# Kernel optimization log

Hardware: AMD Instinct MI355X
Metric: run time of the kernel (lower is better)

The kernel has to match this reference:

```python
import jax, jax.numpy as jnp
import numpy as np
import math

B, S, D, H = 2, 2048, 1024, 16

def setup_inputs() -> dict:
    key = jax.random.key(0)
    ks = jax.random.split(key, 13)
    def lin(kw, kb, out_d, in_d):
        W = jax.random.normal(kw, (out_d, in_d), dtype=jnp.float32) * 0.02
        b = jax.random.normal(kb, (out_d,), dtype=jnp.float32) * 0.02
        return W, b
    Wq, bq = lin(ks[0], ks[1], D, D)
    Wk, bk = lin(ks[2], ks[3], D, D)
    Wv, bv = lin(ks[4], ks[5], D, D)
    Wo, bo = lin(ks[6], ks[7], D, D)
    query = jax.random.normal(ks[8], (B, S, D), dtype=jnp.float32)
    key_t = jax.random.normal(ks[9], (B, S, D), dtype=jnp.float32)
    value = jax.random.normal(ks[10], (B, S, D), dtype=jnp.float32)
    src_mask = jax.random.randint(ks[11], (B, S), 0, 2).astype(bool)  # True = masked out
    return {"query": query, "key": key_t, "value": value, "src_mask": src_mask,
            "Wq": Wq, "bq": bq, "Wk": Wk, "bk": bk, "Wv": Wv, "bv": bv,
            "Wo": Wo, "bo": bo, "nhead": H}

def reference(query, key, value, src_mask, Wq, bq, Wk, bk, Wv, bv, Wo, bo, nhead):
    b, s, d = query.shape
    hd = d // nhead
    scale = 1.0 / math.sqrt(hd)
    def split_heads(x):  # [b,s,d] -> [b,h,s,hd]
        return x.reshape(b, -1, nhead, hd).transpose(0, 2, 1, 3)
    q = split_heads(query @ Wq.T + bq)
    k = split_heads(key @ Wk.T + bk)
    v = split_heads(value @ Wv.T + bv)
    scores = jnp.einsum('bhqe,bhke->bhqk', q, k) * scale  # [b,h,s,s]
    # mask True -> -9e9, broadcast over heads and query positions (matches repeat)
    scores = jnp.where(src_mask[:, None, None, :], jnp.float32(-9e9), scores)
    probs = jax.nn.softmax(scores, axis=-1)
    # dropout is identity in eval mode
    out = jnp.einsum('bhqk,bhke->bhqe', probs, v)  # [b,h,s,hd]
    out = out.transpose(0, 2, 1, 3).reshape(b, s, d)
    out = out @ Wo.T + bo
    return out
```

## Files before the change

kernel.cpp:

```cpp
#include <hip/hip_runtime.h>
#include <hip/hip_bf16.h>
#include <cstdint>
#include <cstddef>

#define B_ 2
#define S_ 2048
#define D_ 1024
#define H_ 16
#define HD_ 64
#define M_ 4096

typedef __attribute__((ext_vector_type(8))) short short8;
typedef __attribute__((ext_vector_type(4))) short shortx4;
typedef __attribute__((ext_vector_type(4))) float floatx4;

__device__ __forceinline__ floatx4 mfma32(short8 a, short8 b, floatx4 c) {
    return __builtin_amdgcn_mfma_f32_16x16x32_bf16(a, b, c, 0, 0, 0);
}
__device__ __forceinline__ floatx4 mfma16(shortx4 a, shortx4 b, floatx4 c) {
    return __builtin_amdgcn_mfma_f32_16x16x16bf16_1k(a, b, c, 0, 0, 0);
}

__device__ __forceinline__ void gload_lds16(const __hip_bfloat16* g, __hip_bfloat16* lds_base) {
    __builtin_amdgcn_global_load_lds(
        (const __attribute__((address_space(1))) void*)g,
        (__attribute__((address_space(3))) void*)lds_base, 16, 0, 0);
}

__global__ __launch_bounds__(256) void cvt3_kernel(
    const float* __restrict__ a, const float* __restrict__ b, const float* __restrict__ c,
    __hip_bfloat16* __restrict__ dst, int n)
{
    const float* src = blockIdx.z == 0 ? a : blockIdx.z == 1 ? b : c;
    __hip_bfloat16* d = dst + (size_t)blockIdx.z * n;
    int i = (blockIdx.x * 256 + threadIdx.x) * 4;
    float4 v = *(const float4*)(src + i);
    union { __hip_bfloat16 h[4]; uint2 u; } cv;
    cv.h[0] = __float2bfloat16(v.x); cv.h[1] = __float2bfloat16(v.y);
    cv.h[2] = __float2bfloat16(v.z); cv.h[3] = __float2bfloat16(v.w);
    *(uint2*)(d + i) = cv.u;
}

__global__ __launch_bounds__(256) void cvt4_kernel(
    const float* __restrict__ a, const float* __restrict__ b,
    const float* __restrict__ c, const float* __restrict__ e,
    __hip_bfloat16* __restrict__ dst, int n)
{
    const float* src = blockIdx.z == 0 ? a : blockIdx.z == 1 ? b : blockIdx.z == 2 ? c : e;
    __hip_bfloat16* d = dst + (size_t)blockIdx.z * n;
    int i = (blockIdx.x * 256 + threadIdx.x) * 4;
    float4 v = *(const float4*)(src + i);
    union { __hip_bfloat16 h[4]; uint2 u; } cv;
    cv.h[0] = __float2bfloat16(v.x); cv.h[1] = __float2bfloat16(v.y);
    cv.h[2] = __float2bfloat16(v.z); cv.h[3] = __float2bfloat16(v.w);
    *(uint2*)(d + i) = cv.u;
}

template <int MODE>
__device__ __forceinline__ void gemm_core(
    const __hip_bfloat16* __restrict__ A,
    const __hip_bfloat16* __restrict__ W,
    const float* __restrict__ bias,
    void* __restrict__ Cout,
    __hip_bfloat16* __restrict__ smem,
    int m0, int n0, int N)
{
    __hip_bfloat16* As = smem;
    __hip_bfloat16* Bs = smem + 128 * 32;
    const int K = D_;
    const int tid  = threadIdx.x;
    const int wave = tid >> 6;
    const int lane = tid & 63;
    const int quad = lane >> 4;
    const int l15  = lane & 15;
    const int wm   = (wave & 1) * 64;
    const int wn   = (wave >> 1) * 64;
    const int srow = lane >> 2;
    const int scol = (lane & 3) * 8;

    floatx4 acc[4][4];
#pragma unroll
    for (int i = 0; i < 4; i++)
#pragma unroll
        for (int j = 0; j < 4; j++) {
            floatx4 z = {0.f, 0.f, 0.f, 0.f};
            acc[i][j] = z;
        }

    for (int k0 = 0; k0 < K; k0 += 32) {
        __syncthreads();
#pragma unroll
        for (int t = 0; t < 2; t++) {
            int r0 = wave * 32 + t * 16;
            gload_lds16(A + (size_t)(m0 + r0 + srow) * K + k0 + scol, As + r0 * 32);
            gload_lds16(W + (size_t)(n0 + r0 + srow) * K + k0 + scol, Bs + r0 * 32);
        }
        __syncthreads();

        short8 afr[4], bfr[4];
#pragma unroll
        for (int i = 0; i < 4; i++)
            afr[i] = *(const short8*)(As + (wm + i * 16 + l15) * 32 + quad * 8);
#pragma unroll
        for (int j = 0; j < 4; j++)
            bfr[j] = *(const short8*)(Bs + (wn + j * 16 + l15) * 32 + quad * 8);
#pragma unroll
        for (int i = 0; i < 4; i++)
#pragma unroll
            for (int j = 0; j < 4; j++)
                acc[i][j] = mfma32(afr[i], bfr[j], acc[i][j]);
    }

    if constexpr (MODE == 1) {
#pragma unroll
        for (int j = 0; j < 4; j++) {
            int col = n0 + wn + j * 16 + l15;
            int h = col >> 6, e = col & 63;
            float bv = bias[col];
#pragma unroll
            for (int i = 0; i < 4; i++) {
                int s0 = m0 + wm + i * 16 + quad * 4;
                int bb = s0 >> 11, sl = s0 & 2047;
                union { __hip_bfloat16 hx[4]; uint2 u; } pk;
#pragma unroll
                for (int r = 0; r < 4; r++)
                    pk.hx[r] = __float2bfloat16(acc[i][j][r] + bv);
                *(uint2*)((__hip_bfloat16*)Cout + (((size_t)bb * H_ + h) * HD_ + e) * S_ + sl) = pk.u;
            }
        }
    } else {
#pragma unroll
        for (int j = 0; j < 4; j++) {
            int col = n0 + wn + j * 16 + l15;
            float bv = bias[col];
#pragma unroll
            for (int i = 0; i < 4; i++) {
#pragma unroll
                for (int r = 0; r < 4; r++) {
                    int rowg = m0 + wm + i * 16 + quad * 4 + r;
                    ((__hip_bfloat16*)Cout)[(size_t)rowg * N + col] =
                        __float2bfloat16(acc[i][j][r] + bv);
                }
            }
        }
    }
}

__global__ __launch_bounds__(256) void qkv_gemm_kernel(
    const __hip_bfloat16* __restrict__ qb, const __hip_bfloat16* __restrict__ kb,
    const __hip_bfloat16* __restrict__ vb,
    const __hip_bfloat16* __restrict__ Wqb, const __hip_bfloat16* __restrict__ Wkb,
    const __hip_bfloat16* __restrict__ Wvb,
    const float* __restrict__ bq, const float* __restrict__ bk, const float* __restrict__ bv,
    __hip_bfloat16* __restrict__ Qp, __hip_bfloat16* __restrict__ Kp,
    __hip_bfloat16* __restrict__ Vt)
{
    __shared__ __hip_bfloat16 smem[2 * 128 * 32] __attribute__((aligned(16)));
    const int z = blockIdx.z;
    const __hip_bfloat16* A = z == 0 ? qb : z == 1 ? kb : vb;
    const __hip_bfloat16* W = z == 0 ? Wqb : z == 1 ? Wkb : Wvb;
    const float* bias = z == 0 ? bq : z == 1 ? bk : bv;
    int m0 = blockIdx.y * 128, n0 = blockIdx.x * 128;
    if (z < 2) gemm_core<0>(A, W, bias, z == 0 ? (void*)Qp : (void*)Kp, smem, m0, n0, D_);
    else       gemm_core<1>(A, W, bias, (void*)Vt, smem, m0, n0, D_);
}

__global__ __launch_bounds__(256) void oproj_gemm_kernel(
    const __hip_bfloat16* __restrict__ A, const __hip_bfloat16* __restrict__ W,
    const float* __restrict__ bias, float* __restrict__ out)
{
    __shared__ __hip_bfloat16 As[64 * 32]  __attribute__((aligned(16)));
    __shared__ __hip_bfloat16 Bs[128 * 32] __attribute__((aligned(16)));
    const int K = D_, N = D_;
    const int tid  = threadIdx.x;
    const int m0   = blockIdx.y * 64;
    const int n0   = blockIdx.x * 128;
    const int wave = tid >> 6;
    const int lane = tid & 63;
    const int quad = lane >> 4;
    const int l15  = lane & 15;
    const int wm   = (wave & 1) * 32;
    const int wn   = (wave >> 1) * 64;
    const int srow = lane >> 2;
    const int scol = (lane & 3) * 8;

    floatx4 acc[2][4];
#pragma unroll
    for (int i = 0; i < 2; i++)
#pragma unroll
        for (int j = 0; j < 4; j++) {
            floatx4 z = {0.f, 0.f, 0.f, 0.f};
            acc[i][j] = z;
        }

    for (int k0 = 0; k0 < K; k0 += 32) {
        __syncthreads();
        {
            int ra = wave * 16;
            gload_lds16(A + (size_t)(m0 + ra + srow) * K + k0 + scol, As + ra * 32);
#pragma unroll
            for (int t = 0; t < 2; t++) {
                int rb = wave * 32 + t * 16;
                gload_lds16(W + (size_t)(n0 + rb + srow) * K + k0 + scol, Bs + rb * 32);
            }
        }
        __syncthreads();

        short8 afr[2], bfr[4];
#pragma unroll
        for (int i = 0; i < 2; i++)
            afr[i] = *(const short8*)(As + (wm + i * 16 + l15) * 32 + quad * 8);
#pragma unroll
        for (int j = 0; j < 4; j++)
            bfr[j] = *(const short8*)(Bs + (wn + j * 16 + l15) * 32 + quad * 8);
#pragma unroll
        for (int i = 0; i < 2; i++)
#pragma unroll
            for (int j = 0; j < 4; j++)
                acc[i][j] = mfma32(afr[i], bfr[j], acc[i][j]);
    }

#pragma unroll
    for (int j = 0; j < 4; j++) {
        int col = n0 + wn + j * 16 + l15;
        float bv = bias[col];
#pragma unroll
        for (int i = 0; i < 2; i++) {
#pragma unroll
            for (int r = 0; r < 4; r++) {
                int rowg = m0 + wm + i * 16 + quad * 4 + r;
                out[(size_t)rowg * N + col] = acc[i][j][r] + bv;
            }
        }
    }
}

#define LDP 72
__global__ __launch_bounds__(512) void flash_attn_kernel(
    const __hip_bfloat16* __restrict__ Q,
    const __hip_bfloat16* __restrict__ Kp,
    const __hip_bfloat16* __restrict__ Vt,
    const int* __restrict__ mask,
    __hip_bfloat16* __restrict__ O)
{
    __shared__ __hip_bfloat16 Qs [128 * LDP] __attribute__((aligned(16)));
    __shared__ __hip_bfloat16 Ks [64 * LDP]  __attribute__((aligned(16)));
    __shared__ __hip_bfloat16 Vts[64 * LDP]  __attribute__((aligned(16)));

    const int tid  = threadIdx.x;
    const int q0   = blockIdx.x * 128;
    const int bh   = blockIdx.y;
    const int b    = bh >> 4;
    const int h    = bh & 15;
    const int wave = tid >> 6;
    const int lane = tid & 63;
    const int quad = lane >> 4;
    const int l15  = lane & 15;
    const float kSc = 0.18033688f;

    const size_t baseQ = ((size_t)b * S_ + q0) * D_ + (size_t)h * HD_;
#pragma unroll
    for (int c = tid; c < 1024; c += 512) {
        int row = c >> 3, kc = c & 7;
        *(uint4*)(Qs + row * LDP + kc * 8) = *(const uint4*)(Q + baseQ + (size_t)row * D_ + kc * 8);
    }
    __syncthreads();

    short8 qb[2];
    qb[0] = *(const short8*)(Qs + (wave * 16 + l15) * LDP + quad * 8);
    qb[1] = *(const short8*)(Qs + (wave * 16 + l15) * LDP + 32 + quad * 8);

    float lsum = 0.f;
    floatx4 o_acc[4];
#pragma unroll
    for (int ot = 0; ot < 4; ot++) {
        floatx4 z = {0.f, 0.f, 0.f, 0.f};
        o_acc[ot] = z;
    }

    const int* mrow = mask + b * S_;
    const __hip_bfloat16* VtBase = Vt + (size_t)bh * HD_ * S_;

    for (int kv0 = 0; kv0 < S_; kv0 += 64) {
        __syncthreads();
        const size_t baseK = ((size_t)b * S_ + kv0) * D_ + (size_t)h * HD_;
        {
            int row = tid >> 3, kc = tid & 7;
            *(uint4*)(Ks + row * LDP + kc * 8) =
                *(const uint4*)(Kp + baseK + (size_t)row * D_ + kc * 8);
            *(uint4*)(Vts + row * LDP + kc * 8) =
                *(const uint4*)(VtBase + (size_t)row * S_ + kv0 + kc * 8);
        }
        __syncthreads();

        int4 mq[4];
#pragma unroll
        for (int nt = 0; nt < 4; nt++)
            mq[nt] = *(const int4*)(mrow + kv0 + nt * 16 + quad * 4);

        floatx4 s_acc[4];
#pragma unroll
        for (int nt = 0; nt < 4; nt++) {
            short8 kb0 = *(const short8*)(Ks + (nt * 16 + l15) * LDP + quad * 8);
            short8 kb1 = *(const short8*)(Ks + (nt * 16 + l15) * LDP + 32 + quad * 8);
            floatx4 z = {0.f, 0.f, 0.f, 0.f};
            z = mfma32(kb0, qb[0], z);
            z = mfma32(kb1, qb[1], z);
            s_acc[nt] = z;
        }

        shortx4 pf[4];
#pragma unroll
        for (int nt = 0; nt < 4; nt++) {
            float pe0 = mq[nt].x ? 0.f : __builtin_amdgcn_exp2f(s_acc[nt][0] * kSc);
            float pe1 = mq[nt].y ? 0.f : __builtin_amdgcn_exp2f(s_acc[nt][1] * kSc);
            float pe2 = mq[nt].z ? 0.f : __builtin_amdgcn_exp2f(s_acc[nt][2] * kSc);
            float pe3 = mq[nt].w ? 0.f : __builtin_amdgcn_exp2f(s_acc[nt][3] * kSc);
            lsum += (pe0 + pe1) + (pe2 + pe3);
            union { shortx4 s4; __hip_bfloat162 b2[2]; } pk;
            pk.b2[0] = __float22bfloat162_rn({pe0, pe1});
            pk.b2[1] = __float22bfloat162_rn({pe2, pe3});
            pf[nt] = pk.s4;
        }

#pragma unroll
        for (int nt = 0; nt < 4; nt++) {
#pragma unroll
            for (int ot = 0; ot < 4; ot++) {
                shortx4 vb = *(const shortx4*)(Vts + (ot * 16 + l15) * LDP + nt * 16 + quad * 4);
                o_acc[ot] = mfma16(pf[nt], vb, o_acc[ot]);
            }
        }
    }

    lsum += __shfl_xor(lsum, 16);
    lsum += __shfl_xor(lsum, 32);

    const size_t baseO = ((size_t)b * S_ + q0) * D_ + (size_t)h * HD_;
#pragma unroll
    for (int r = 0; r < 4; r++) {
        float inv = 1.0f / __shfl(lsum, quad * 4 + r);
        int rowl = wave * 16 + quad * 4 + r;
#pragma unroll
        for (int ot = 0; ot < 4; ot++)
            O[baseO + (size_t)rowl * D_ + ot * 16 + l15] =
                __float2bfloat16(o_acc[ot][r] * inv);
    }
}

extern "C" void kernel_launch(void* const* d_in, const int* in_sizes, int n_in,
                              void* d_out, int out_size, void* d_ws, size_t ws_size,
                              hipStream_t stream) {
    const float* query = (const float*)d_in[0];
    const float* key   = (const float*)d_in[1];
    const float* value = (const float*)d_in[2];
    const int*   mask  = (const int*)d_in[3];
    const float* Wq    = (const float*)d_in[4];
    const float* bq    = (const float*)d_in[5];
    const float* Wk    = (const float*)d_in[6];
    const float* bk    = (const float*)d_in[7];
    const float* Wv    = (const float*)d_in[8];
    const float* bv    = (const float*)d_in[9];
    const float* Wo    = (const float*)d_in[10];
    const float* bo    = (const float*)d_in[11];
    float* out = (float*)d_out;

    const size_t SZ_IN = (size_t)M_ * D_;
    const size_t SZ_W  = (size_t)D_ * D_;
    __hip_bfloat16* qb  = (__hip_bfloat16*)d_ws;
    __hip_bfloat16* kb  = qb  + SZ_IN;
    __hip_bfloat16* vb  = kb  + SZ_IN;
    __hip_bfloat16* Wqb = vb  + SZ_IN;
    __hip_bfloat16* Wkb = Wqb + SZ_W;
    __hip_bfloat16* Wvb = Wkb + SZ_W;
    __hip_bfloat16* Wob = Wvb + SZ_W;
    __hip_bfloat16* Qp  = Wob + SZ_W;
    __hip_bfloat16* Kp  = Qp  + SZ_IN;
    __hip_bfloat16* Vt  = Kp  + SZ_IN;

    cvt3_kernel<<<dim3(SZ_IN / 1024, 1, 3), 256, 0, stream>>>(query, key, value, qb, (int)SZ_IN);
    cvt4_kernel<<<dim3(SZ_W / 1024, 1, 4), 256, 0, stream>>>(Wq, Wk, Wv, Wo, Wqb, (int)SZ_W);

    qkv_gemm_kernel<<<dim3(D_ / 128, M_ / 128, 3), 256, 0, stream>>>(
        qb, kb, vb, Wqb, Wkb, Wvb, bq, bk, bv, Qp, Kp, Vt);

    flash_attn_kernel<<<dim3(S_ / 128, B_ * H_), 512, 0, stream>>>(Qp, Kp, Vt, mask, Qp);

    oproj_gemm_kernel<<<dim3(D_ / 128, M_ / 64), 256, 0, stream>>>(Qp, Wob, bo, out);
}
```

Before: 239.5 us.

## Fold softmax scale into Q projection, MFMA row sums, merge conversions

Merges the input and weight fp32-to-bf16 conversion kernels into one launch. Moves the softmax scale (including the log2e factor) into the Q projection epilogue, so the attention loop exponentiates raw scores. Replaces the per-lane VALU row-sum accumulation and final shuffles with an MFMA against a ones vector, which sums the bf16-rounded probabilities. This trades VALU work for one extra matrix op per tile and adds a slight change in rounding.

```diff
diff --git a/kernel.cpp b/kernel.cpp
--- a/kernel.cpp
+++ b/kernel.cpp
@@ -27,33 +27,33 @@
         (__attribute__((address_space(3))) void*)lds_base, 16, 0, 0);
 }
 
-__global__ __launch_bounds__(256) void cvt3_kernel(
-    const float* __restrict__ a, const float* __restrict__ b, const float* __restrict__ c,
-    __hip_bfloat16* __restrict__ dst, int n)
-{
-    const float* src = blockIdx.z == 0 ? a : blockIdx.z == 1 ? b : c;
-    __hip_bfloat16* d = dst + (size_t)blockIdx.z * n;
+__global__ __launch_bounds__(256) void cvt_all_kernel(
+    const float* __restrict__ q, const float* __restrict__ k, const float* __restrict__ v,
+    const float* __restrict__ wq, const float* __restrict__ wk,
+    const float* __restrict__ wv, const float* __restrict__ wo,
+    __hip_bfloat16* __restrict__ dst_in,
+    __hip_bfloat16* __restrict__ dst_w)
+{
+    const size_t SZ_IN = (size_t)M_ * D_;
+    const size_t SZ_W  = (size_t)D_ * D_;
     int i = (blockIdx.x * 256 + threadIdx.x) * 4;
-    float4 v = *(const float4*)(src + i);
+    const float* src;
+    __hip_bfloat16* d;
+    if (blockIdx.z < 3) {
+        src = blockIdx.z == 0 ? q : blockIdx.z == 1 ? k : v;
+        d = dst_in + (size_t)blockIdx.z * SZ_IN + i;
+        src += i;
+    } else {
+        int w = i >> 20;
+        int off = i & (int)(SZ_W - 1);
+        src = (w == 0 ? wq : w == 1 ? wk : w == 2 ? wv : wo) + off;
+        d = dst_w + (size_t)w * SZ_W + off;
+    }
+    float4 vv = *(const float4*)src;
     union { __hip_bfloat16 h[4]; uint2 u; } cv;
-    cv.h[0] = __float2bfloat16(v.x); cv.h[1] = __float2bfloat16(v.y);
-    cv.h[2] = __float2bfloat16(v.z); cv.h[3] = __float2bfloat16(v.w);
-    *(uint2*)(d + i) = cv.u;
-}
-
-__global__ __launch_bounds__(256) void cvt4_kernel(
-    const float* __restrict__ a, const float* __restrict__ b,
-    const float* __restrict__ c, const float* __restrict__ e,
-    __hip_bfloat16* __restrict__ dst, int n)
-{
-    const float* src = blockIdx.z == 0 ? a : blockIdx.z == 1 ? b : blockIdx.z == 2 ? c : e;
-    __hip_bfloat16* d = dst + (size_t)blockIdx.z * n;
-    int i = (blockIdx.x * 256 + threadIdx.x) * 4;
-    float4 v = *(const float4*)(src + i);
-    union { __hip_bfloat16 h[4]; uint2 u; } cv;
-    cv.h[0] = __float2bfloat16(v.x); cv.h[1] = __float2bfloat16(v.y);
-    cv.h[2] = __float2bfloat16(v.z); cv.h[3] = __float2bfloat16(v.w);
-    *(uint2*)(d + i) = cv.u;
+    cv.h[0] = __float2bfloat16(vv.x); cv.h[1] = __float2bfloat16(vv.y);
+    cv.h[2] = __float2bfloat16(vv.z); cv.h[3] = __float2bfloat16(vv.w);
+    *(uint2*)d = cv.u;
 }
 
 template <int MODE>
@@ -63,7 +63,7 @@
     const float* __restrict__ bias,
     void* __restrict__ Cout,
     __hip_bfloat16* __restrict__ smem,
-    int m0, int n0, int N)
+    int m0, int n0, int N, float scale)
 {
     __hip_bfloat16* As = smem;
     __hip_bfloat16* Bs = smem + 128 * 32;
@@ -139,7 +139,7 @@
                 for (int r = 0; r < 4; r++) {
                     int rowg = m0 + wm + i * 16 + quad * 4 + r;
                     ((__hip_bfloat16*)Cout)[(size_t)rowg * N + col] =
-                        __float2bfloat16(acc[i][j][r] + bv);
+                        __float2bfloat16((acc[i][j][r] + bv) * scale);
                 }
             }
         }
@@ -161,8 +161,10 @@
     const __hip_bfloat16* W = z == 0 ? Wqb : z == 1 ? Wkb : Wvb;
     const float* bias = z == 0 ? bq : z == 1 ? bk : bv;
     int m0 = blockIdx.y * 128, n0 = blockIdx.x * 128;
-    if (z < 2) gemm_core<0>(A, W, bias, z == 0 ? (void*)Qp : (void*)Kp, smem, m0, n0, D_);
-    else       gemm_core<1>(A, W, bias, (void*)Vt, smem, m0, n0, D_);
+    const float kSc = 0.18033688f;
+    if (z < 2) gemm_core<0>(A, W, bias, z == 0 ? (void*)Qp : (void*)Kp, smem, m0, n0, D_,
+                            z == 0 ? kSc : 1.0f);
+    else       gemm_core<1>(A, W, bias, (void*)Vt, smem, m0, n0, D_, 1.0f);
 }
 
 __global__ __launch_bounds__(256) void oproj_gemm_kernel(
@@ -256,7 +258,6 @@
     const int lane = tid & 63;
     const int quad = lane >> 4;
     const int l15  = lane & 15;
-    const float kSc = 0.18033688f;
 
     const size_t baseQ = ((size_t)b * S_ + q0) * D_ + (size_t)h * HD_;
 #pragma unroll
@@ -270,7 +271,8 @@
     qb[0] = *(const short8*)(Qs + (wave * 16 + l15) * LDP + quad * 8);
     qb[1] = *(const short8*)(Qs + (wave * 16 + l15) * LDP + 32 + quad * 8);
 
-    float lsum = 0.f;
+    const shortx4 ones = {(short)0x3F80, (short)0x3F80, (short)0x3F80, (short)0x3F80};
+    floatx4 l_acc = {0.f, 0.f, 0.f, 0.f};
     floatx4 o_acc[4];
 #pragma unroll
     for (int ot = 0; ot < 4; ot++) {
@@ -312,11 +314,10 @@
         shortx4 pf[4];
 #pragma unroll
         for (int nt = 0; nt < 4; nt++) {
-            float pe0 = mq[nt].x ? 0.f : __builtin_amdgcn_exp2f(s_acc[nt][0] * kSc);
-            float pe1 = mq[nt].y ? 0.f : __builtin_amdgcn_exp2f(s_acc[nt][1] * kSc);
-            float pe2 = mq[nt].z ? 0.f : __builtin_amdgcn_exp2f(s_acc[nt][2] * kSc);
-            float pe3 = mq[nt].w ? 0.f : __builtin_amdgcn_exp2f(s_acc[nt][3] * kSc);
-            lsum += (pe0 + pe1) + (pe2 + pe3);
+            float pe0 = mq[nt].x ? 0.f : __builtin_amdgcn_exp2f(s_acc[nt][0]);
+            float pe1 = mq[nt].y ? 0.f : __builtin_amdgcn_exp2f(s_acc[nt][1]);
+            float pe2 = mq[nt].z ? 0.f : __builtin_amdgcn_exp2f(s_acc[nt][2]);
+            float pe3 = mq[nt].w ? 0.f : __builtin_amdgcn_exp2f(s_acc[nt][3]);
             union { shortx4 s4; __hip_bfloat162 b2[2]; } pk;
             pk.b2[0] = __float22bfloat162_rn({pe0, pe1});
             pk.b2[1] = __float22bfloat162_rn({pe2, pe3});
@@ -325,6 +326,7 @@
 
 #pragma unroll
         for (int nt = 0; nt < 4; nt++) {
+            l_acc = mfma16(pf[nt], ones, l_acc);
 #pragma unroll
             for (int ot = 0; ot < 4; ot++) {
                 shortx4 vb = *(const shortx4*)(Vts + (ot * 16 + l15) * LDP + nt * 16 + quad * 4);
@@ -333,13 +335,10 @@
         }
     }
 
-    lsum += __shfl_xor(lsum, 16);
-    lsum += __shfl_xor(lsum, 32);
-
     const size_t baseO = ((size_t)b * S_ + q0) * D_ + (size_t)h * HD_;
 #pragma unroll
     for (int r = 0; r < 4; r++) {
-        float inv = 1.0f / __shfl(lsum, quad * 4 + r);
+        float inv = 1.0f / l_acc[r];
         int rowl = wave * 16 + quad * 4 + r;
 #pragma unroll
         for (int ot = 0; ot < 4; ot++)
@@ -378,8 +377,8 @@
     __hip_bfloat16* Kp  = Qp  + SZ_IN;
     __hip_bfloat16* Vt  = Kp  + SZ_IN;
 
-    cvt3_kernel<<<dim3(SZ_IN / 1024, 1, 3), 256, 0, stream>>>(query, key, value, qb, (int)SZ_IN);
-    cvt4_kernel<<<dim3(SZ_W / 1024, 1, 4), 256, 0, stream>>>(Wq, Wk, Wv, Wo, Wqb, (int)SZ_W);
+    cvt_all_kernel<<<dim3(SZ_IN / 1024, 1, 4), 256, 0, stream>>>(
+        query, key, value, Wq, Wk, Wv, Wo, qb, Wqb);
 
     qkv_gemm_kernel<<<dim3(D_ / 128, M_ / 128, 3), 256, 0, stream>>>(
         qb, kb, vb, Wqb, Wkb, Wvb, bq, bk, bv, Qp, Kp, Vt);
```

Result: slower. 247.8 us (+3.5%).
